# Kernel tuning notes

Hardware: AMD Instinct MI355X
Metric: run time of the kernel (lower is better)

## Reference

```python
import jax, jax.numpy as jnp
import numpy as np

B, S, H, HS, D = 256, 16, 8, 128, 1024
M = H * HS  # mem_size = 1024
FORGET_BIAS = 1.0


def setup_inputs() -> dict:
    key = jax.random.key(0)
    ks = jax.random.split(key, 16)
    n = lambda k, shape, s=0.02: (jax.random.normal(k, shape, jnp.float32) * s)
    return {
        'inputs': jax.random.normal(ks[0], (B, D), jnp.float32),
        'h_state': jax.random.normal(ks[1], (B, S, M), jnp.float32),
        'm_state': jax.random.normal(ks[2], (B, S, M), jnp.float32),
        'W_emb': n(ks[3], (D, M)), 'b_emb': jnp.zeros((M,), jnp.float32),
        'W_g': n(ks[4], (M, M)), 'b_g': jnp.zeros((M,), jnp.float32),
        'W_wf': n(ks[5], (D, M)), 'W_wi': n(ks[6], (D, M)), 'W_wo': n(ks[7], (D, M)),
        'W_uf': n(ks[8], (M, M)), 'b_uf': jnp.zeros((M,), jnp.float32),
        'W_ui': n(ks[9], (M, M)), 'b_ui': jnp.zeros((M,), jnp.float32),
        'W_uo': n(ks[10], (M, M)), 'b_uo': jnp.zeros((M,), jnp.float32),
    }


def _rmc_forward(inputs, h_state, m_state, W_emb, b_emb, W_g, b_g,
                 W_wf, W_wi, W_wo, W_uf, b_uf, W_ui, b_ui, W_uo, b_uo):
    # input embedding: [B, D] -> [B, M]
    dense_inputs = inputs @ W_emb + b_emb
    # keys/values: memory with the embedded input appended as an extra slot -> [B, S+1, M]
    kv = jnp.concatenate([m_state, dense_inputs[:, None, :]], axis=1)
    # multi-head scaled dot-product attention (no q/k/v projections in AttentionMap)
    q = m_state.reshape(B, S, H, HS)
    k = kv.reshape(B, S + 1, H, HS)
    v = kv.reshape(B, S + 1, H, HS)
    scores = jnp.einsum('bqhd,bkhd->bhqk', q, k) / jnp.sqrt(jnp.asarray(HS, q.dtype))
    attn = jax.nn.softmax(scores, axis=-1)
    attended = jnp.einsum('bhqk,bkhd->bqhd', attn, v).reshape(B, S, M)

    memory_proposal = m_state + attended
    memory_proposal = (memory_proposal @ W_g + b_g) + memory_proposal

    forget_gate = jax.nn.sigmoid(h_state @ W_uf + b_uf + (inputs @ W_wf)[:, None, :])
    input_gate = jax.nn.sigmoid(h_state @ W_ui + b_ui + (inputs @ W_wi)[:, None, :])
    output_gate = jax.nn.sigmoid(h_state @ W_uo + b_uo + (inputs @ W_wo)[:, None, :])

    # NOTE: faithful to the original (including the sigmoid around m*f + bias and
    # the double-sigmoid on the input/output gates)
    new_memories = jax.nn.sigmoid(m_state * forget_gate + FORGET_BIAS) \
        + memory_proposal * jax.nn.sigmoid(input_gate)
    new_hidden = jnp.tanh(m_state) * jax.nn.sigmoid(output_gate)
    return new_memories, new_hidden


def reference(inputs, h_state, m_state, W_emb, b_emb, W_g, b_g,
              W_wf, W_wi, W_wo, W_uf, b_uf, W_ui, b_ui, W_uo, b_uo):
    return _rmc_forward(inputs, h_state, m_state, W_emb, b_emb, W_g, b_g,
                        W_wf, W_wi, W_wo, W_uf, b_uf, W_ui, b_ui, W_uo, b_uo)
```

## Files before the change

### kernel.cpp

```cpp
#include <hip/hip_runtime.h>
#include <hip/hip_bf16.h>


typedef __hip_bfloat16 bf16;
typedef __bf16 bf16x8 __attribute__((ext_vector_type(8)));
typedef float  f32x4  __attribute__((ext_vector_type(4)));

__device__ __forceinline__ float b2f(bf16 x) { return __bfloat162float(x); }
__device__ __forceinline__ bf16  f2b(float x) { return __float2bfloat16(x); }
__device__ __forceinline__ unsigned short fbits(float x) {
    bf16 b = __float2bfloat16(x);
    return *(unsigned short*)&b;
}
__device__ __forceinline__ float sig(float x) { return 1.0f / (1.0f + __expf(-x)); }
__device__ __forceinline__ float ftanh(float x) {
    return 1.0f - 2.0f / (1.0f + __expf(2.0f * x));
}

__device__ __forceinline__ void gl_lds16(const void* g, void* l) {
    __builtin_amdgcn_global_load_lds(
        (const __attribute__((address_space(1))) void*)g,
        (__attribute__((address_space(3))) void*)l,
        16, 0, 0);
}

__device__ __forceinline__ float4 ld_bf4(const bf16* p) {
    ushort4 u = *(const ushort4*)p;
    float4 r;
    r.x = b2f(*(const bf16*)&u.x);
    r.y = b2f(*(const bf16*)&u.y);
    r.z = b2f(*(const bf16*)&u.z);
    r.w = b2f(*(const bf16*)&u.w);
    return r;
}

__global__ __launch_bounds__(256) void k_prep(
    const float* __restrict__ W_g, const float* __restrict__ W_uf,
    const float* __restrict__ W_ui, const float* __restrict__ W_uo,
    const float* __restrict__ W_emb, const float* __restrict__ W_wf,
    const float* __restrict__ W_wi, const float* __restrict__ W_wo,
    const float* __restrict__ b_emb,
    const float* __restrict__ h_state, const float* __restrict__ inputs,
    bf16* __restrict__ wt, bf16* __restrict__ hbf, float* __restrict__ proj)
{
    __shared__ __align__(16) char sbuf[32768];
    const int blk = blockIdx.x;
    const int tid = threadIdx.x;

    if (blk < 64) {
        const float* Wsrc4[4] = {W_emb, W_wf, W_wi, W_wo};
        const int by = blk >> 5, bx = blk & 31;
        const int which = bx >> 3;
        const int n0 = (bx & 7) * 128;
        const int m0 = by * 128;
        const float* Wsrc = Wsrc4[which];
        char* LA = sbuf;
        char* LB = sbuf + 16384;

        const int wv = tid >> 6, lane = tid & 63;
        const int mrow = lane & 15, q = lane >> 4;
        const int rb = (wv & 1) * 64, cb = (wv >> 1) * 64;

        const f32x4 zero4 = {0.0f, 0.0f, 0.0f, 0.0f};
        f32x4 acc[4][4];
        #pragma unroll
        for (int i = 0; i < 4; ++i)
            #pragma unroll
            for (int j = 0; j < 4; ++j) acc[i][j] = zero4;

        for (int k0 = 0; k0 < 1024; k0 += 64) {
            #pragma unroll
            for (int r = 0; r < 8; ++r) {
                int lin = r * 256 + tid;
                int row = lin >> 4, f4 = lin & 15;
                float4 v = *(const float4*)(inputs + (size_t)(m0 + row) * 1024 + k0 + f4 * 4);
                ushort4 p;
                p.x = fbits(v.x); p.y = fbits(v.y); p.z = fbits(v.z); p.w = fbits(v.w);
                *(ushort4*)(LA + row * 128 + ((f4 * 8) ^ ((row & 7) << 4))) = p;
            }
            #pragma unroll
            for (int r = 0; r < 2; ++r) {
                int lin = r * 256 + tid;
                int kq = lin >> 5, cq = lin & 31;
                const float* wp = Wsrc + (size_t)(k0 + kq * 4) * 1024 + n0 + cq * 4;
                float4 v0 = *(const float4*)(wp);
                float4 v1 = *(const float4*)(wp + 1024);
                float4 v2 = *(const float4*)(wp + 2048);
                float4 v3 = *(const float4*)(wp + 3072);
                const float* e0 = (const float*)&v0;
                const float* e1 = (const float*)&v1;
                const float* e2 = (const float*)&v2;
                const float* e3 = (const float*)&v3;
                #pragma unroll
                for (int j = 0; j < 4; ++j) {
                    int c = cq * 4 + j;
                    ushort4 p;
                    p.x = fbits(e0[j]); p.y = fbits(e1[j]);
                    p.z = fbits(e2[j]); p.w = fbits(e3[j]);
                    *(ushort4*)(LB + c * 128 + ((kq * 8) ^ ((c & 7) << 4))) = p;
                }
            }
            __syncthreads();
            #pragma unroll
            for (int kk = 0; kk < 2; ++kk) {
                const int kb = kk * 64 + q * 16;
                bf16x8 afr[4], bfr[4];
                #pragma unroll
                for (int i = 0; i < 4; ++i) {
                    int row = rb + i * 16 + mrow;
                    afr[i] = *(const bf16x8*)(LA + row * 128 + (kb ^ ((row & 7) << 4)));
                }
                #pragma unroll
                for (int j = 0; j < 4; ++j) {
                    int n = cb + j * 16 + mrow;
                    bfr[j] = *(const bf16x8*)(LB + n * 128 + (kb ^ ((n & 7) << 4)));
                }
                #pragma unroll
                for (int i = 0; i < 4; ++i)
                    #pragma unroll
                    for (int j = 0; j < 4; ++j)
                        acc[i][j] = __builtin_amdgcn_mfma_f32_16x16x32_bf16(afr[i], bfr[j], acc[i][j], 0, 0, 0);
            }
            __syncthreads();
        }
        float* P = proj + which * 262144;
        #pragma unroll
        for (int j = 0; j < 4; ++j) {
            const int colp = n0 + cb + j * 16 + mrow;
            const float bias = (which == 0) ? b_emb[colp] : 0.0f;
            #pragma unroll
            for (int i = 0; i < 4; ++i)
                #pragma unroll
                for (int r = 0; r < 4; ++r) {
                    const int row = m0 + rb + i * 16 + q * 4 + r;
                    P[(size_t)row * 1024 + colp] = acc[i][j][r] + bias;
                }
        }
    } else if (blk < 4160) {
        const float* Ws[4] = {W_g, W_uf, W_ui, W_uo};
        const int t = blk - 64;
        const int plane = t >> 10;
        const int tt = t & 1023;
        const int nb = (tt & 31) * 32, kb2 = (tt >> 5) * 32;
        const float* W = Ws[plane];
        bf16* Wt = wt + (size_t)plane * (1024 * 1024);
        float (*tl)[33] = (float (*)[33])sbuf;
        const int tx = tid & 31, ty = tid >> 5;
        #pragma unroll
        for (int r = 0; r < 4; ++r)
            tl[r * 8 + ty][tx] = W[(size_t)(kb2 + r * 8 + ty) * 1024 + nb + tx];
        __syncthreads();
        #pragma unroll
        for (int r = 0; r < 4; ++r)
            Wt[(size_t)(nb + r * 8 + ty) * 1024 + kb2 + tx] = f2b(tl[tx][r * 8 + ty]);
    } else {
        const int e = blk - 4160;
        int idx = (e * 256 + tid) * 8;
        #pragma unroll
        for (int half = 0; half < 2; ++half) {
            float4 v = *(const float4*)(h_state + idx + half * 4);
            hbf[idx + half * 4 + 0] = f2b(v.x);
            hbf[idx + half * 4 + 1] = f2b(v.y);
            hbf[idx + half * 4 + 2] = f2b(v.z);
            hbf[idx + half * 4 + 3] = f2b(v.w);
        }
    }
}

__global__ __launch_bounds__(256) void k_attn(
    const float* __restrict__ m_state,
    const float* __restrict__ dense,
    bf16* __restrict__ mp)
{
    const int b = blockIdx.x >> 3;
    const int h = blockIdx.x & 7;
    const int tid = threadIdx.x;

    __shared__ float kv[17][132];
    __shared__ float sc[16][18];

    for (int idx = tid; idx < 17 * 32; idx += 256) {
        int r = idx >> 5, d4 = idx & 31;
        const float* src = (r < 16)
            ? &m_state[(size_t)(b * 16 + r) * 1024 + h * 128 + d4 * 4]
            : &dense[(size_t)b * 1024 + h * 128 + d4 * 4];
        float4 v = *(const float4*)src;
        *(float4*)&kv[r][d4 * 4] = v;
    }
    __syncthreads();

    for (int p = tid; p < 16 * 17; p += 256) {
        int qi = p / 17, ki = p % 17;
        float dx = 0.f, dy = 0.f, dz = 0.f, dw = 0.f;
        #pragma unroll 8
        for (int d4 = 0; d4 < 32; ++d4) {
            float4 a = *(const float4*)&kv[qi][d4 * 4];
            float4 c = *(const float4*)&kv[ki][d4 * 4];
            dx += a.x * c.x; dy += a.y * c.y; dz += a.z * c.z; dw += a.w * c.w;
        }
        sc[qi][ki] = (dx + dy + dz + dw) * 0.0883883476483184f;
    }
    __syncthreads();

    if (tid < 16) {
        float mx = -1e30f;
        for (int k = 0; k < 17; ++k) mx = fmaxf(mx, sc[tid][k]);
        float s = 0.0f;
        for (int k = 0; k < 17; ++k) { float e = __expf(sc[tid][k] - mx); sc[tid][k] = e; s += e; }
        float inv = 1.0f / s;
        for (int k = 0; k < 17; ++k) sc[tid][k] *= inv;
    }
    __syncthreads();

    for (int p = tid; p < 16 * 32; p += 256) {
        int qi = p >> 5, d4 = p & 31;
        float sx = 0.f, sy = 0.f, sz = 0.f, sw = 0.f;
        #pragma unroll
        for (int k = 0; k < 17; ++k) {
            float w = sc[qi][k];
            float4 v = *(const float4*)&kv[k][d4 * 4];
            sx += w * v.x; sy += w * v.y; sz += w * v.z; sw += w * v.w;
        }
        float4 base = *(const float4*)&kv[qi][d4 * 4];
        size_t off = (size_t)(b * 16 + qi) * 1024 + h * 128 + d4 * 4;
        mp[off + 0] = f2b(base.x + sx);
        mp[off + 1] = f2b(base.y + sy);
        mp[off + 2] = f2b(base.z + sz);
        mp[off + 3] = f2b(base.w + sw);
    }
}

__global__ __launch_bounds__(512, 2) void k_gemm_big(
    const bf16* __restrict__ hbf,
    const bf16* __restrict__ mpb,
    const bf16* __restrict__ wt,
    bf16* __restrict__ pre,
    bf16* __restrict__ preg)
{
    extern __shared__ __align__(16) char smem[];

    int bid = blockIdx.x;
    bid = (bid & 7) * 32 + (bid >> 3);
    const int by = bid & 15;
    const int ct = bid >> 4;
    const int m0 = by * 256;

    const bf16* A; const bf16* Bp; bf16* Cout; int bn0;
    if (ct < 12) {
        A = hbf;
        const int g = ct >> 2;
        bn0 = (ct & 3) * 256;
        Bp = wt + (size_t)(1 + g) * (1024 * 1024);
        Cout = pre + (size_t)g * (4096 * 1024);
    } else {
        A = mpb;
        bn0 = (ct - 12) * 256;
        Bp = wt;
        Cout = preg;
    }

    const int wv = threadIdx.x >> 6;
    const int lane = threadIdx.x & 63;
    const int r8 = lane >> 3, c8 = lane & 7;
    const int mrow = lane & 15, q = lane >> 4;
    const int wr = wv >> 2, wc = wv & 3;

    const f32x4 zero4 = {0.0f, 0.0f, 0.0f, 0.0f};
    f32x4 acc[8][4];
    #pragma unroll
    for (int i = 0; i < 8; ++i)
        #pragma unroll
        for (int j = 0; j < 4; ++j) acc[i][j] = zero4;

    auto STAGE = [&](int buf, int k0) {
        char* sA = smem + buf * 65536;
        char* sB = sA + 32768;
        #pragma unroll
        for (int t = 0; t < 4; ++t) {
            const int rr = wv * 32 + t * 8;
            gl_lds16(A  + (size_t)(m0  + rr + r8) * 1024 + k0 + (c8 ^ r8) * 8, sA + rr * 128);
            gl_lds16(Bp + (size_t)(bn0 + rr + r8) * 1024 + k0 + (c8 ^ r8) * 8, sB + rr * 128);
        }
    };

    STAGE(0, 0);

    #pragma unroll 2
    for (int step = 0; step < 16; ++step) {
        const int cur = step & 1;
        if (step < 15) {
            STAGE(cur ^ 1, (step + 1) * 64);
            asm volatile("s_waitcnt vmcnt(8)" ::: "memory");
        } else {
            asm volatile("s_waitcnt vmcnt(0)" ::: "memory");
        }
        __builtin_amdgcn_s_barrier();
        __builtin_amdgcn_sched_barrier(0);

        const char* sA = smem + cur * 65536;
        const char* sB = sA + 32768;
        #pragma unroll
        for (int kk = 0; kk < 2; ++kk) {
            const int kb = kk * 64 + q * 16;
            bf16x8 afr[8], bfr[4];
            #pragma unroll
            for (int i = 0; i < 8; ++i) {
                const int row = wr * 128 + i * 16 + mrow;
                afr[i] = *(const bf16x8*)(sA + row * 128 + (kb ^ ((row & 7) << 4)));
            }
            #pragma unroll
            for (int j = 0; j < 4; ++j) {
                const int n = wc * 64 + j * 16 + mrow;
                bfr[j] = *(const bf16x8*)(sB + n * 128 + (kb ^ ((n & 7) << 4)));
            }
            #pragma unroll
            for (int i = 0; i < 8; ++i)
                #pragma unroll
                for (int j = 0; j < 4; ++j)
                    acc[i][j] = __builtin_amdgcn_mfma_f32_16x16x32_bf16(afr[i], bfr[j], acc[i][j], 0, 0, 0);
        }
        __builtin_amdgcn_sched_barrier(0);
        __builtin_amdgcn_s_barrier();
    }

    #pragma unroll
    for (int j = 0; j < 4; ++j) {
        const int col = bn0 + wc * 64 + j * 16 + mrow;
        #pragma unroll
        for (int i = 0; i < 8; ++i)
            #pragma unroll
            for (int r = 0; r < 4; ++r) {
                const int row = m0 + wr * 128 + i * 16 + q * 4 + r;
                Cout[(size_t)row * 1024 + col] = f2b(acc[i][j][r]);
            }
    }
}

__global__ __launch_bounds__(256) void k_epi(
    const float* __restrict__ m_state,
    const bf16* __restrict__ mpb,
    const bf16* __restrict__ preg,
    const bf16* __restrict__ pre,
    const float* __restrict__ proj,
    const float* __restrict__ b_g, const float* __restrict__ b_uf,
    const float* __restrict__ b_ui, const float* __restrict__ b_uo,
    float* __restrict__ out_mem, float* __restrict__ out_hid)
{
    const int idx = (blockIdx.x * 256 + threadIdx.x) * 4;
    const int row = idx >> 10;
    const int col = idx & 1023;
    const int b = row >> 4;

    float4 m4  = *(const float4*)(m_state + idx);
    float4 mp4 = ld_bf4(mpb + idx);
    float4 pg4 = ld_bf4(preg + idx);
    float4 pf4 = ld_bf4(pre + idx);
    float4 pi4 = ld_bf4(pre + 4194304 + idx);
    float4 po4 = ld_bf4(pre + 8388608 + idx);
    float4 xf4 = *(const float4*)(proj + 262144 + b * 1024 + col);
    float4 xi4 = *(const float4*)(proj + 524288 + b * 1024 + col);
    float4 xo4 = *(const float4*)(proj + 786432 + b * 1024 + col);
    float4 bg4 = *(const float4*)(b_g + col);
    float4 bf4 = *(const float4*)(b_uf + col);
    float4 bi4 = *(const float4*)(b_ui + col);
    float4 bo4 = *(const float4*)(b_uo + col);

    float4 om, oh;
    {
        float mp2 = pg4.x + bg4.x + mp4.x;
        float fg = sig(pf4.x + bf4.x + xf4.x);
        float ig = sig(pi4.x + bi4.x + xi4.x);
        float og = sig(po4.x + bo4.x + xo4.x);
        om.x = sig(m4.x * fg + 1.0f) + mp2 * sig(ig);
        oh.x = ftanh(m4.x) * sig(og);
    }
    {
        float mp2 = pg4.y + bg4.y + mp4.y;
        float fg = sig(pf4.y + bf4.y + xf4.y);
        float ig = sig(pi4.y + bi4.y + xi4.y);
        float og = sig(po4.y + bo4.y + xo4.y);
        om.y = sig(m4.y * fg + 1.0f) + mp2 * sig(ig);
        oh.y = ftanh(m4.y) * sig(og);
    }
    {
        float mp2 = pg4.z + bg4.z + mp4.z;
        float fg = sig(pf4.z + bf4.z + xf4.z);
        float ig = sig(pi4.z + bi4.z + xi4.z);
        float og = sig(po4.z + bo4.z + xo4.z);
        om.z = sig(m4.z * fg + 1.0f) + mp2 * sig(ig);
        oh.z = ftanh(m4.z) * sig(og);
    }
    {
        float mp2 = pg4.w + bg4.w + mp4.w;
        float fg = sig(pf4.w + bf4.w + xf4.w);
        float ig = sig(pi4.w + bi4.w + xi4.w);
        float og = sig(po4.w + bo4.w + xo4.w);
        om.w = sig(m4.w * fg + 1.0f) + mp2 * sig(ig);
        oh.w = ftanh(m4.w) * sig(og);
    }

    *(float4*)(out_mem + idx) = om;
    *(float4*)(out_hid + idx) = oh;
}

extern "C" void kernel_launch(void* const* d_in, const int* in_sizes, int n_in,
                              void* d_out, int out_size, void* d_ws, size_t ws_size,
                              hipStream_t stream)
{
    const float* inputs  = (const float*)d_in[0];
    const float* h_state = (const float*)d_in[1];
    const float* m_state = (const float*)d_in[2];
    const float* W_emb   = (const float*)d_in[3];
    const float* b_emb   = (const float*)d_in[4];
    const float* W_g     = (const float*)d_in[5];
    const float* b_g     = (const float*)d_in[6];
    const float* W_wf    = (const float*)d_in[7];
    const float* W_wi    = (const float*)d_in[8];
    const float* W_wo    = (const float*)d_in[9];
    const float* W_uf    = (const float*)d_in[10];
    const float* b_uf    = (const float*)d_in[11];
    const float* W_ui    = (const float*)d_in[12];
    const float* b_ui    = (const float*)d_in[13];
    const float* W_uo    = (const float*)d_in[14];
    const float* b_uo    = (const float*)d_in[15];

    char* wsb = (char*)d_ws;
    float* proj = (float*)wsb;
    bf16*  hbf  = (bf16*)(wsb + 4u  * 1048576u);
    bf16*  mpb  = (bf16*)(wsb + 12u * 1048576u);
    bf16*  wt   = (bf16*)(wsb + 20u * 1048576u);
    bf16*  pre  = (bf16*)(wsb + 28u * 1048576u);
    bf16*  preg = (bf16*)(wsb + 52u * 1048576u);

    float* out_mem = (float*)d_out;
    float* out_hid = out_mem + (size_t)4096 * 1024;

    k_prep<<<dim3(6208), dim3(256), 0, stream>>>(
        W_g, W_uf, W_ui, W_uo, W_emb, W_wf, W_wi, W_wo, b_emb,
        h_state, inputs, wt, hbf, proj);

    k_attn<<<dim3(256 * 8), dim3(256), 0, stream>>>(m_state, proj, mpb);

    k_gemm_big<<<dim3(256), dim3(512), 131072, stream>>>(hbf, mpb, wt, pre, preg);

    k_epi<<<dim3(4096), dim3(256), 0, stream>>>(
        m_state, mpb, preg, pre, proj,
        b_g, b_uf, b_ui, b_uo, out_mem, out_hid);
}
```

Before: 233.9 us.

## Split-K the input projection GEMMs and widen transpose/convert tiles in prep kernel

Result: faster. 218.8 us (-6.5%).

```diff
diff --git a/kernel.cpp b/kernel.cpp
--- a/kernel.cpp
+++ b/kernel.cpp
@@ -5,6 +5,7 @@
 typedef __hip_bfloat16 bf16;
 typedef __bf16 bf16x8 __attribute__((ext_vector_type(8)));
 typedef float  f32x4  __attribute__((ext_vector_type(4)));
+typedef unsigned short u16x8 __attribute__((ext_vector_type(8)));
 
 __device__ __forceinline__ float b2f(bf16 x) { return __bfloat162float(x); }
 __device__ __forceinline__ bf16  f2b(float x) { return __float2bfloat16(x); }
@@ -39,20 +40,22 @@
     const float* __restrict__ W_ui, const float* __restrict__ W_uo,
     const float* __restrict__ W_emb, const float* __restrict__ W_wf,
     const float* __restrict__ W_wi, const float* __restrict__ W_wo,
-    const float* __restrict__ b_emb,
     const float* __restrict__ h_state, const float* __restrict__ inputs,
-    bf16* __restrict__ wt, bf16* __restrict__ hbf, float* __restrict__ proj)
+    bf16* __restrict__ wt, bf16* __restrict__ hbf, float* __restrict__ part)
 {
     __shared__ __align__(16) char sbuf[32768];
     const int blk = blockIdx.x;
     const int tid = threadIdx.x;
 
-    if (blk < 64) {
+    if (blk < 128) {
         const float* Wsrc4[4] = {W_emb, W_wf, W_wi, W_wo};
-        const int by = blk >> 5, bx = blk & 31;
-        const int which = bx >> 3;
-        const int n0 = (bx & 7) * 128;
-        const int m0 = by * 128;
+        const int ks = blk & 1;
+        const int nt = (blk >> 1) & 31;
+        const int mt = blk >> 6;
+        const int which = nt >> 3;
+        const int n0 = (nt & 7) * 128;
+        const int m0 = mt * 128;
+        const int kbase = ks * 512;
         const float* Wsrc = Wsrc4[which];
         char* LA = sbuf;
         char* LB = sbuf + 16384;
@@ -68,7 +71,8 @@
             #pragma unroll
             for (int j = 0; j < 4; ++j) acc[i][j] = zero4;
 
-        for (int k0 = 0; k0 < 1024; k0 += 64) {
+        for (int s = 0; s < 8; ++s) {
+            const int k0 = kbase + s * 64;
             #pragma unroll
             for (int r = 0; r < 8; ++r) {
                 int lin = r * 256 + tid;
@@ -123,53 +127,65 @@
             }
             __syncthreads();
         }
-        float* P = proj + which * 262144;
+        float* P = part + ((size_t)(ks * 4 + which) * 256) * 1024;
         #pragma unroll
         for (int j = 0; j < 4; ++j) {
             const int colp = n0 + cb + j * 16 + mrow;
-            const float bias = (which == 0) ? b_emb[colp] : 0.0f;
             #pragma unroll
             for (int i = 0; i < 4; ++i)
                 #pragma unroll
                 for (int r = 0; r < 4; ++r) {
                     const int row = m0 + rb + i * 16 + q * 4 + r;
-                    P[(size_t)row * 1024 + colp] = acc[i][j][r] + bias;
+                    P[(size_t)row * 1024 + colp] = acc[i][j][r];
                 }
         }
-    } else if (blk < 4160) {
+    } else if (blk < 1152) {
         const float* Ws[4] = {W_g, W_uf, W_ui, W_uo};
-        const int t = blk - 64;
-        const int plane = t >> 10;
-        const int tt = t & 1023;
-        const int nb = (tt & 31) * 32, kb2 = (tt >> 5) * 32;
+        const int t = blk - 128;
+        const int plane = t >> 8;
+        const int tt = t & 255;
+        const int kb = (tt >> 4) * 64;
+        const int nb = (tt & 15) * 64;
         const float* W = Ws[plane];
         bf16* Wt = wt + (size_t)plane * (1024 * 1024);
-        float (*tl)[33] = (float (*)[33])sbuf;
-        const int tx = tid & 31, ty = tid >> 5;
-        #pragma unroll
-        for (int r = 0; r < 4; ++r)
-            tl[r * 8 + ty][tx] = W[(size_t)(kb2 + r * 8 + ty) * 1024 + nb + tx];
+        float (*tl)[65] = (float (*)[65])sbuf;
+
+        #pragma unroll
+        for (int it = 0; it < 4; ++it) {
+            int lin = it * 256 + tid;
+            int kr = lin >> 4, n4 = lin & 15;
+            *(float4*)&tl[kr][n4 * 4] =
+                *(const float4*)(W + (size_t)(kb + kr) * 1024 + nb + n4 * 4);
+        }
         __syncthreads();
         #pragma unroll
-        for (int r = 0; r < 4; ++r)
-            Wt[(size_t)(nb + r * 8 + ty) * 1024 + kb2 + tx] = f2b(tl[tx][r * 8 + ty]);
+        for (int it = 0; it < 2; ++it) {
+            int lin = it * 256 + tid;
+            int n = lin >> 3, k8 = (lin & 7) * 8;
+            u16x8 p;
+            #pragma unroll
+            for (int j = 0; j < 8; ++j) p[j] = fbits(tl[k8 + j][n]);
+            *(u16x8*)(Wt + (size_t)(nb + n) * 1024 + kb + k8) = p;
+        }
     } else {
-        const int e = blk - 4160;
-        int idx = (e * 256 + tid) * 8;
-        #pragma unroll
-        for (int half = 0; half < 2; ++half) {
-            float4 v = *(const float4*)(h_state + idx + half * 4);
-            hbf[idx + half * 4 + 0] = f2b(v.x);
-            hbf[idx + half * 4 + 1] = f2b(v.y);
-            hbf[idx + half * 4 + 2] = f2b(v.z);
-            hbf[idx + half * 4 + 3] = f2b(v.w);
+        const int e = blk - 1152;
+        size_t idx = ((size_t)e * 256 + tid) * 16;
+        #pragma unroll
+        for (int hh = 0; hh < 2; ++hh) {
+            float4 a = *(const float4*)(h_state + idx + hh * 8);
+            float4 b = *(const float4*)(h_state + idx + hh * 8 + 4);
+            u16x8 p;
+            p[0] = fbits(a.x); p[1] = fbits(a.y); p[2] = fbits(a.z); p[3] = fbits(a.w);
+            p[4] = fbits(b.x); p[5] = fbits(b.y); p[6] = fbits(b.z); p[7] = fbits(b.w);
+            *(u16x8*)(hbf + idx + hh * 8) = p;
         }
     }
 }
 
 __global__ __launch_bounds__(256) void k_attn(
     const float* __restrict__ m_state,
-    const float* __restrict__ dense,
+    const float* __restrict__ part,
+    const float* __restrict__ b_emb,
     bf16* __restrict__ mp)
 {
     const int b = blockIdx.x >> 3;
@@ -181,10 +197,18 @@
 
     for (int idx = tid; idx < 17 * 32; idx += 256) {
         int r = idx >> 5, d4 = idx & 31;
-        const float* src = (r < 16)
-            ? &m_state[(size_t)(b * 16 + r) * 1024 + h * 128 + d4 * 4]
-            : &dense[(size_t)b * 1024 + h * 128 + d4 * 4];
-        float4 v = *(const float4*)src;
+        float4 v;
+        if (r < 16) {
+            v = *(const float4*)&m_state[(size_t)(b * 16 + r) * 1024 + h * 128 + d4 * 4];
+        } else {
+            float4 v0 = *(const float4*)&part[(size_t)b * 1024 + h * 128 + d4 * 4];
+            float4 v1 = *(const float4*)&part[(size_t)(4 * 256 + b) * 1024 + h * 128 + d4 * 4];
+            float4 be = *(const float4*)&b_emb[h * 128 + d4 * 4];
+            v.x = v0.x + v1.x + be.x;
+            v.y = v0.y + v1.y + be.y;
+            v.z = v0.z + v1.z + be.z;
+            v.w = v0.w + v1.w + be.w;
+        }
         *(float4*)&kv[r][d4 * 4] = v;
     }
     __syncthreads();
@@ -341,7 +365,7 @@
     const bf16* __restrict__ mpb,
     const bf16* __restrict__ preg,
     const bf16* __restrict__ pre,
-    const float* __restrict__ proj,
+    const float* __restrict__ part,
     const float* __restrict__ b_g, const float* __restrict__ b_uf,
     const float* __restrict__ b_ui, const float* __restrict__ b_uo,
     float* __restrict__ out_mem, float* __restrict__ out_hid)
@@ -357,9 +381,19 @@
     float4 pf4 = ld_bf4(pre + idx);
     float4 pi4 = ld_bf4(pre + 4194304 + idx);
     float4 po4 = ld_bf4(pre + 8388608 + idx);
-    float4 xf4 = *(const float4*)(proj + 262144 + b * 1024 + col);
-    float4 xi4 = *(const float4*)(proj + 524288 + b * 1024 + col);
-    float4 xo4 = *(const float4*)(proj + 786432 + b * 1024 + col);
+
+    const size_t po = (size_t)b * 1024 + col;
+    float4 xfa = *(const float4*)(part + 262144 + po);
+    float4 xfb = *(const float4*)(part + 1048576 + 262144 + po);
+    float4 xia = *(const float4*)(part + 524288 + po);
+    float4 xib = *(const float4*)(part + 1048576 + 524288 + po);
+    float4 xoa = *(const float4*)(part + 786432 + po);
+    float4 xob = *(const float4*)(part + 1048576 + 786432 + po);
+    float4 xf4, xi4, xo4;
+    xf4.x = xfa.x + xfb.x; xf4.y = xfa.y + xfb.y; xf4.z = xfa.z + xfb.z; xf4.w = xfa.w + xfb.w;
+    xi4.x = xia.x + xib.x; xi4.y = xia.y + xib.y; xi4.z = xia.z + xib.z; xi4.w = xia.w + xib.w;
+    xo4.x = xoa.x + xob.x; xo4.y = xoa.y + xob.y; xo4.z = xoa.z + xob.z; xo4.w = xoa.w + xob.w;
+
     float4 bg4 = *(const float4*)(b_g + col);
     float4 bf4 = *(const float4*)(b_uf + col);
     float4 bi4 = *(const float4*)(b_ui + col);
@@ -425,25 +459,25 @@
     const float* b_uo    = (const float*)d_in[15];
 
     char* wsb = (char*)d_ws;
-    float* proj = (float*)wsb;
-    bf16*  hbf  = (bf16*)(wsb + 4u  * 1048576u);
-    bf16*  mpb  = (bf16*)(wsb + 12u * 1048576u);
-    bf16*  wt   = (bf16*)(wsb + 20u * 1048576u);
-    bf16*  pre  = (bf16*)(wsb + 28u * 1048576u);
-    bf16*  preg = (bf16*)(wsb + 52u * 1048576u);
+    float* part = (float*)wsb;
+    bf16*  hbf  = (bf16*)(wsb + 8u  * 1048576u);
+    bf16*  mpb  = (bf16*)(wsb + 16u * 1048576u);
+    bf16*  wt   = (bf16*)(wsb + 24u * 1048576u);
+    bf16*  pre  = (bf16*)(wsb + 32u * 1048576u);
+    bf16*  preg = (bf16*)(wsb + 56u * 1048576u);
 
     float* out_mem = (float*)d_out;
     float* out_hid = out_mem + (size_t)4096 * 1024;
 
-    k_prep<<<dim3(6208), dim3(256), 0, stream>>>(
-        W_g, W_uf, W_ui, W_uo, W_emb, W_wf, W_wi, W_wo, b_emb,
-        h_state, inputs, wt, hbf, proj);
-
-    k_attn<<<dim3(256 * 8), dim3(256), 0, stream>>>(m_state, proj, mpb);
+    k_prep<<<dim3(2176), dim3(256), 0, stream>>>(
+        W_g, W_uf, W_ui, W_uo, W_emb, W_wf, W_wi, W_wo,
+        h_state, inputs, wt, hbf, part);
+
+    k_attn<<<dim3(256 * 8), dim3(256), 0, stream>>>(m_state, part, b_emb, mpb);
 
     k_gemm_big<<<dim3(256), dim3(512), 131072, stream>>>(hbf, mpb, wt, pre, preg);
 
     k_epi<<<dim3(4096), dim3(256), 0, stream>>>(
-        m_state, mpb, preg, pre, proj,
+        m_state, mpb, preg, pre, part,
         b_g, b_uf, b_ui, b_uo, out_mem, out_hid);
 }
```
